# Kernel tuning notes

Measured on AMD Instinct MI355X. Metric: run time of the kernel, lower is better.

Reference implementation:

```python
import jax, jax.numpy as jnp
import numpy as np


def _hungarian(cost):
    """Jonker-Volgenant shortest-augmenting-path LAP solver (minimum cost).

    Returns col_ind such that rows arange(n) are matched to columns col_ind,
    identical (in objective) to scipy.optimize.linear_sum_assignment.
    Runs on host numpy, mirroring the original's detach().cpu() + scipy path.
    """
    cost = np.asarray(cost, dtype=np.float64)
    n = cost.shape[0]
    INF = np.inf
    u = np.zeros(n + 1)
    v = np.zeros(n + 1)
    p = np.zeros(n + 1, dtype=np.int64)   # p[j]: row (1-based) assigned to column j
    way = np.zeros(n + 1, dtype=np.int64)
    for i in range(1, n + 1):
        p[0] = i
        j0 = 0
        minv = np.full(n + 1, INF)
        used = np.zeros(n + 1, dtype=bool)
        while True:
            used[j0] = True
            i0 = p[j0]
            # vectorized relaxation of reduced costs for all unused columns
            cur = cost[i0 - 1] - u[i0] - v[1:]
            free = ~used[1:]
            upd = free & (cur < minv[1:])
            minv[1:] = np.where(upd, cur, minv[1:])
            way[1:] = np.where(upd, j0, way[1:])
            cand = np.where(free, minv[1:], INF)
            j1 = int(np.argmin(cand)) + 1
            delta = cand[j1 - 1]
            u[p[used]] += delta
            v[used] -= delta
            minv[1:] = np.where(free, minv[1:] - delta, minv[1:])
            j0 = j1
            if p[j0] == 0:
                break
        # augment along the alternating path
        while j0:
            j1 = way[j0]
            p[j0] = p[j1]
            j0 = j1
    col = np.empty(n, dtype=np.int64)
    col[p[1:] - 1] = np.arange(n)
    return col


def setup_inputs() -> dict:
    key = jax.random.key(0)
    B, N = 64, 256
    D = jax.random.normal(key, (B, N, N), dtype=jnp.float32)
    return {"D": D}


def reference(D):
    # Host round-trip for the assignment, exactly as the torch module does
    # (D.detach().cpu().numpy() -> scipy LAP per batch element).
    Dn = np.asarray(jax.device_get(D))
    cols = np.stack([_hungarian(Dn[b]) for b in range(Dn.shape[0])])  # [B, N]
    idx = jnp.asarray(cols)[:, :, None]                               # [B, N, 1]
    # gather matched costs D[b, i, col[b, i]] and reduce: mean per batch, then mean
    matched = jnp.take_along_axis(D, idx, axis=2)[..., 0]             # [B, N]
    return matched.mean(axis=1).mean()
```

## Files before the change

kernel.cpp:

```cpp
#include <hip/hip_runtime.h>
#include <hip/hip_fp16.h>

#define N_DIM 256
#define BATCH 64
#define BS 64

struct __align__(8) H4 { __half2 a, b; };

__device__ __forceinline__ unsigned fmap(float f) {
    unsigned b = __float_as_uint(f);
    return (b & 0x80000000u) ? ~b : (b | 0x80000000u);
}

#define DPP_MINU(x, ctrl) do {                                                 \
    unsigned _s = (unsigned)__builtin_amdgcn_update_dpp((int)(x), (int)(x),    \
                                                        (ctrl), 0xf, 0xf, false); \
    (x) = ((x) < _s) ? (x) : _s;                                               \
} while (0)

__device__ __forceinline__ unsigned wave_min_u32(unsigned x) {
    DPP_MINU(x, 0x111); DPP_MINU(x, 0x112); DPP_MINU(x, 0x114); DPP_MINU(x, 0x118);
    DPP_MINU(x, 0x142); DPP_MINU(x, 0x143);
    return (unsigned)__builtin_amdgcn_readlane((int)x, 63);
}

__device__ __forceinline__ int rd4_i(int x0, int x1, int x2, int x3, int idx) {
    const int sel = idx & 3, src = idx >> 2;
    int ab = (sel & 1) ? x1 : x0;
    int cd = (sel & 1) ? x3 : x2;
    int vv = (sel & 2) ? cd : ab;
    return __builtin_amdgcn_readlane(vv, src);
}
__device__ __forceinline__ float rd4_f(float x0, float x1, float x2, float x3, int idx) {
    return __int_as_float(rd4_i(__float_as_int(x0), __float_as_int(x1),
                                __float_as_int(x2), __float_as_int(x3), idx));
}

#define SET4(x0, x1, x2, x3, idx, val) do {                                    \
    const int _sel = (idx) & 3;                                                \
    if (t == ((idx) >> 2)) {                                                   \
        if (_sel == 0) x0 = (val); else if (_sel == 1) x1 = (val);             \
        else if (_sel == 2) x2 = (val); else x3 = (val);                       \
    }                                                                          \
} while (0)

__global__ __launch_bounds__(BS) void lap_kernel(const float* __restrict__ Dm,
                                                 double* __restrict__ batch_sums) {
    const int b = blockIdx.x;
    const int t = threadIdx.x;
    const float* __restrict__ cost = Dm + (size_t)b * N_DIM * N_DIM;
    const float4* __restrict__ cost4 = (const float4*)cost;

    __shared__ H4       ch[N_DIM * BS];
    __shared__ float    u_s[N_DIM];
    __shared__ float    v_s[N_DIM];
    __shared__ int      row4col_s[N_DIM];
    __shared__ int      col4row_s[N_DIM];
    __shared__ int      queue_s[N_DIM];
    __shared__ unsigned bid_s[N_DIM];
    __shared__ int      qcnt_s;

    const int c0i = 4 * t, c1i = 4 * t + 1, c2i = 4 * t + 2, c3i = 4 * t + 3;

    float cmn0 = INFINITY, cmn1 = INFINITY, cmn2 = INFINITY, cmn3 = INFINITY;
    int   ca0 = 0, ca1 = 0, ca2 = 0, ca3 = 0;
    for (int r = 0; r < N_DIM; ++r) {
        const float4 c4 = cost4[r * BS + t];
        H4 h;
        h.a = __floats2half2_rn(c4.x, c4.y);
        h.b = __floats2half2_rn(c4.z, c4.w);
        ch[r * BS + t] = h;
        const float r0 = __low2float(h.a), r1 = __high2float(h.a);
        const float r2 = __low2float(h.b), r3 = __high2float(h.b);
        if (r0 < cmn0) { cmn0 = r0; ca0 = r; }
        if (r1 < cmn1) { cmn1 = r1; ca1 = r; }
        if (r2 < cmn2) { cmn2 = r2; ca2 = r; }
        if (r3 < cmn3) { cmn3 = r3; ca3 = r; }
    }
    {
        float4 vv; vv.x = cmn0; vv.y = cmn1; vv.z = cmn2; vv.w = cmn3;
        ((float4*)v_s)[t] = vv;
        float4 zz; zz.x = 0.f; zz.y = 0.f; zz.z = 0.f; zz.w = 0.f;
        ((float4*)u_s)[t] = zz;
        int4 mm; mm.x = -1; mm.y = -1; mm.z = -1; mm.w = -1;
        ((int4*)row4col_s)[t] = mm;
        ((int4*)col4row_s)[t] = mm;
        int4 rc; rc.x = 0x7fffffff; rc.y = 0x7fffffff; rc.z = 0x7fffffff; rc.w = 0x7fffffff;
        ((int4*)queue_s)[t] = rc;
        uint4 bb; bb.x = ~0u; bb.y = ~0u; bb.z = ~0u; bb.w = ~0u;
        ((uint4*)bid_s)[t] = bb;
    }
    __syncthreads();
    atomicMin(&queue_s[ca0], c0i);
    atomicMin(&queue_s[ca1], c1i);
    atomicMin(&queue_s[ca2], c2i);
    atomicMin(&queue_s[ca3], c3i);
    __syncthreads();
    if (queue_s[ca0] == c0i) { row4col_s[c0i] = ca0; col4row_s[ca0] = c0i; }
    if (queue_s[ca1] == c1i) { row4col_s[c1i] = ca1; col4row_s[ca1] = c1i; }
    if (queue_s[ca2] == c2i) { row4col_s[c2i] = ca2; col4row_s[ca2] = c2i; }
    if (queue_s[ca3] == c3i) { row4col_s[c3i] = ca3; col4row_s[ca3] = c3i; }
    __syncthreads();

    for (int pass = 0; pass < 12; ++pass) {
        if (t == 0) qcnt_s = 0;
        __syncthreads();
        {
            const int4 my = ((const int4*)col4row_s)[t];
            const int nf = (my.x < 0) + (my.y < 0) + (my.z < 0) + (my.w < 0);
            if (nf) {
                int pos = atomicAdd(&qcnt_s, nf);
                if (my.x < 0) queue_s[pos++] = c0i;
                if (my.y < 0) queue_s[pos++] = c1i;
                if (my.z < 0) queue_s[pos++] = c2i;
                if (my.w < 0) queue_s[pos++] = c3i;
            }
        }
        __syncthreads();
        const int n = qcnt_s;
        if (n == 0) break;
        const int my_row = (t < n) ? queue_s[t] : -1;
        float d1 = INFINITY, d2 = INFINITY;
        int   j1 = 0;
        if (my_row >= 0) {
            const int base = my_row * BS;
            for (int l = 0; l < BS; ++l) {
                const int l2 = (l + t) & 63;
                const H4 h = ch[base + l2];
                const float4 vv = ((const float4*)v_s)[l2];
                float d;
                d = __low2float(h.a)  - vv.x; if (d < d1) { d2 = d1; d1 = d; j1 = 4 * l2 + 0; } else if (d < d2) d2 = d;
                d = __high2float(h.a) - vv.y; if (d < d1) { d2 = d1; d1 = d; j1 = 4 * l2 + 1; } else if (d < d2) d2 = d;
                d = __low2float(h.b)  - vv.z; if (d < d1) { d2 = d1; d1 = d; j1 = 4 * l2 + 2; } else if (d < d2) d2 = d;
                d = __high2float(h.b) - vv.w; if (d < d1) { d2 = d1; d1 = d; j1 = 4 * l2 + 3; } else if (d < d2) d2 = d;
            }
            atomicMin(&bid_s[j1], (fmap(d1) & 0xFFFFFF00u) | (unsigned)t);
        }
        __syncthreads();
        if (my_row >= 0) {
            const unsigned mybid = (fmap(d1) & 0xFFFFFF00u) | (unsigned)t;
            if (bid_s[j1] == mybid) {
                const int i0 = row4col_s[j1];
                row4col_s[j1] = my_row;
                col4row_s[my_row] = j1;
                if (i0 >= 0) col4row_s[i0] = -1;
                u_s[my_row] = d2;
                v_s[j1] += d1 - d2;
                bid_s[j1] = ~0u;
            }
        }
        __syncthreads();
    }

    const float4 vv4 = ((const float4*)v_s)[t];
    float v0 = vv4.x, v1 = vv4.y, v2 = vv4.z, v3 = vv4.w;
    const int4 m4 = ((const int4*)row4col_s)[t];
    int r4c0 = m4.x, r4c1 = m4.y, r4c2 = m4.z, r4c3 = m4.w;
    const int4 y4 = ((const int4*)col4row_s)[t];
    int c4r0 = y4.x, c4r1 = y4.y, c4r2 = y4.z, c4r3 = y4.w;
    int p0 = 0, p1 = 0, p2 = 0, p3 = 0;

    unsigned long long fm0 = __ballot(c4r0 < 0);
    unsigned long long fm1 = __ballot(c4r1 < 0);
    unsigned long long fm2 = __ballot(c4r2 < 0);
    unsigned long long fm3 = __ballot(c4r3 < 0);

    const unsigned KINF0 = (fmap(INFINITY) & 0xFFFFFF00u) | (unsigned)c0i;
    const unsigned KINF1 = (fmap(INFINITY) & 0xFFFFFF00u) | (unsigned)c1i;
    const unsigned KINF2 = (fmap(INFINITY) & 0xFFFFFF00u) | (unsigned)c2i;
    const unsigned KINF3 = (fmap(INFINITY) & 0xFFFFFF00u) | (unsigned)c3i;

    while (fm0 | fm1 | fm2 | fm3) {
        int i;
        if (fm0)      { const int tt = __builtin_ctzll(fm0); fm0 &= fm0 - 1; i = tt * 4 + 0; }
        else if (fm1) { const int tt = __builtin_ctzll(fm1); fm1 &= fm1 - 1; i = tt * 4 + 1; }
        else if (fm2) { const int tt = __builtin_ctzll(fm2); fm2 &= fm2 - 1; i = tt * 4 + 2; }
        else          { const int tt = __builtin_ctzll(fm3); fm3 &= fm3 - 1; i = tt * 4 + 3; }

        float spc0 = INFINITY, spc1 = INFINITY, spc2 = INFINITY, spc3 = INFINITY;
        unsigned key0 = KINF0, key1 = KINF1, key2 = KINF2, key3 = KINF3;
        int   scan = 0;
        int   cur = i;
        float minVal = 0.0f;
        int   sink = -1;

        while (true) {
            const H4    h = ch[cur * BS + t];
            const float ucur = u_s[cur];
            const float add = minVal - ucur;

            float r;
            r = add + __low2float(h.a)  - v0;
            if (r < spc0) { spc0 = r; p0 = cur; key0 = (fmap(r) & 0xFFFFFF00u) | (unsigned)c0i; }
            r = add + __high2float(h.a) - v1;
            if (r < spc1) { spc1 = r; p1 = cur; key1 = (fmap(r) & 0xFFFFFF00u) | (unsigned)c1i; }
            r = add + __low2float(h.b)  - v2;
            if (r < spc2) { spc2 = r; p2 = cur; key2 = (fmap(r) & 0xFFFFFF00u) | (unsigned)c2i; }
            r = add + __high2float(h.b) - v3;
            if (r < spc3) { spc3 = r; p3 = cur; key3 = (fmap(r) & 0xFFFFFF00u) | (unsigned)c3i; }

            unsigned k01 = (key0 < key1) ? key0 : key1;
            unsigned k23 = (key2 < key3) ? key2 : key3;
            const unsigned gk = wave_min_u32((k01 < k23) ? k01 : k23);
            const int bi = (int)(gk & 0xFFu);

            const float mv = rd4_f(spc0, spc1, spc2, spc3, bi);
            const int   r4 = rd4_i(r4c0, r4c1, r4c2, r4c3, bi);
            minVal = mv;
            if (t == (bi >> 2)) {
                const int s = bi & 3;
                scan |= 1 << s;
                if (s == 0) key0 = ~0u; else if (s == 1) key1 = ~0u;
                else if (s == 2) key2 = ~0u; else key3 = ~0u;
            }
            if (r4 < 0) { sink = bi; break; }
            cur = r4;
        }

        if (scan & 1) { const float dv = minVal - spc0; v0 -= dv; if (r4c0 >= 0) u_s[r4c0] += dv; }
        if (scan & 2) { const float dv = minVal - spc1; v1 -= dv; if (r4c1 >= 0) u_s[r4c1] += dv; }
        if (scan & 4) { const float dv = minVal - spc2; v2 -= dv; if (r4c2 >= 0) u_s[r4c2] += dv; }
        if (scan & 8) { const float dv = minVal - spc3; v3 -= dv; if (r4c3 >= 0) u_s[r4c3] += dv; }
        if (t == 0) u_s[i] += minVal;

        if (sink >= 0) {
            int jj = sink;
            while (true) {
                const int ii = rd4_i(p0, p1, p2, p3, jj);
                SET4(r4c0, r4c1, r4c2, r4c3, jj, ii);
                const int tmp = rd4_i(c4r0, c4r1, c4r2, c4r3, ii);
                SET4(c4r0, c4r1, c4r2, c4r3, ii, jj);
                jj = tmp;
                if (ii == i) break;
            }
        }
    }

    double s = 0.0;
    s += (double)cost[(size_t)(t * 4 + 0) * N_DIM + c4r0];
    s += (double)cost[(size_t)(t * 4 + 1) * N_DIM + c4r1];
    s += (double)cost[(size_t)(t * 4 + 2) * N_DIM + c4r2];
    s += (double)cost[(size_t)(t * 4 + 3) * N_DIM + c4r3];
    #pragma unroll
    for (int off = 32; off > 0; off >>= 1) s += __shfl_down(s, off);
    if (t == 0) batch_sums[b] = s;
}

__global__ void finalize_kernel(const double* __restrict__ batch_sums,
                                float* __restrict__ out) {
    const int t = threadIdx.x;
    double s = batch_sums[t];
    #pragma unroll
    for (int off = 32; off > 0; off >>= 1) s += __shfl_down(s, off);
    if (t == 0) out[0] = (float)(s / (double)((long long)BATCH * N_DIM));
}

extern "C" void kernel_launch(void* const* d_in, const int* in_sizes, int n_in,
                              void* d_out, int out_size, void* d_ws, size_t ws_size,
                              hipStream_t stream) {
    const float* Dm = (const float*)d_in[0];
    float* out = (float*)d_out;
    double* sums = (double*)d_ws;

    lap_kernel<<<BATCH, BS, 0, stream>>>(Dm, sums);
    finalize_kernel<<<1, 64, 0, stream>>>(sums, out);
}
```

Measured before the change: 906.8 us.

## Switch LAP solver to scaled 16-bit fixed-point integer costs and duals

Replaces the fp16 cost cache and float duals with costs scaled by 4096, rounded to int16 and packed in pairs, plus integer duals. The shortest-path inner loop now packs the reduced cost and column index into one integer key, so the per-step readlane of the min value and the fmap conversions go away. The auction pass now processes queued rows in chunks of 64 instead of only the first 64. It risks overflow or clipping for large costs and changes rounding versus the fp16 version, which could alter the chosen assignment.

```diff
diff --git a/kernel.cpp b/kernel.cpp
--- a/kernel.cpp
+++ b/kernel.cpp
@@ -1,16 +1,9 @@
 #include <hip/hip_runtime.h>
-#include <hip/hip_fp16.h>
 
 #define N_DIM 256
 #define BATCH 64
 #define BS 64
-
-struct __align__(8) H4 { __half2 a, b; };
-
-__device__ __forceinline__ unsigned fmap(float f) {
-    unsigned b = __float_as_uint(f);
-    return (b & 0x80000000u) ? ~b : (b | 0x80000000u);
-}
+#define SCALE 4096.0f
 
 #define DPP_MINU(x, ctrl) do {                                                 \
     unsigned _s = (unsigned)__builtin_amdgcn_update_dpp((int)(x), (int)(x),    \
@@ -30,10 +23,6 @@
     int cd = (sel & 1) ? x3 : x2;
     int vv = (sel & 2) ? cd : ab;
     return __builtin_amdgcn_readlane(vv, src);
-}
-__device__ __forceinline__ float rd4_f(float x0, float x1, float x2, float x3, int idx) {
-    return __int_as_float(rd4_i(__float_as_int(x0), __float_as_int(x1),
-                                __float_as_int(x2), __float_as_int(x3), idx));
 }
 
 #define SET4(x0, x1, x2, x3, idx, val) do {                                    \
@@ -44,6 +33,9 @@
     }                                                                          \
 } while (0)
 
+__device__ __forceinline__ int lo16(int p) { return (int)(short)(p & 0xFFFF); }
+__device__ __forceinline__ int hi16(int p) { return p >> 16; }
+
 __global__ __launch_bounds__(BS) void lap_kernel(const float* __restrict__ Dm,
                                                  double* __restrict__ batch_sums) {
     const int b = blockIdx.x;
@@ -51,9 +43,9 @@
     const float* __restrict__ cost = Dm + (size_t)b * N_DIM * N_DIM;
     const float4* __restrict__ cost4 = (const float4*)cost;
 
-    __shared__ H4       ch[N_DIM * BS];
-    __shared__ float    u_s[N_DIM];
-    __shared__ float    v_s[N_DIM];
+    __shared__ int2     chi[N_DIM * BS];
+    __shared__ int      u_s[N_DIM];
+    __shared__ int      v_s[N_DIM];
     __shared__ int      row4col_s[N_DIM];
     __shared__ int      col4row_s[N_DIM];
     __shared__ int      queue_s[N_DIM];
@@ -62,26 +54,28 @@
 
     const int c0i = 4 * t, c1i = 4 * t + 1, c2i = 4 * t + 2, c3i = 4 * t + 3;
 
-    float cmn0 = INFINITY, cmn1 = INFINITY, cmn2 = INFINITY, cmn3 = INFINITY;
-    int   ca0 = 0, ca1 = 0, ca2 = 0, ca3 = 0;
+    int cmn0 = INT_MAX, cmn1 = INT_MAX, cmn2 = INT_MAX, cmn3 = INT_MAX;
+    int ca0 = 0, ca1 = 0, ca2 = 0, ca3 = 0;
     for (int r = 0; r < N_DIM; ++r) {
         const float4 c4 = cost4[r * BS + t];
-        H4 h;
-        h.a = __floats2half2_rn(c4.x, c4.y);
-        h.b = __floats2half2_rn(c4.z, c4.w);
-        ch[r * BS + t] = h;
-        const float r0 = __low2float(h.a), r1 = __high2float(h.a);
-        const float r2 = __low2float(h.b), r3 = __high2float(h.b);
-        if (r0 < cmn0) { cmn0 = r0; ca0 = r; }
-        if (r1 < cmn1) { cmn1 = r1; ca1 = r; }
-        if (r2 < cmn2) { cmn2 = r2; ca2 = r; }
-        if (r3 < cmn3) { cmn3 = r3; ca3 = r; }
+        const int a0 = __float2int_rn(c4.x * SCALE);
+        const int a1 = __float2int_rn(c4.y * SCALE);
+        const int a2 = __float2int_rn(c4.z * SCALE);
+        const int a3 = __float2int_rn(c4.w * SCALE);
+        int2 p;
+        p.x = (a0 & 0xFFFF) | (a1 << 16);
+        p.y = (a2 & 0xFFFF) | (a3 << 16);
+        chi[r * BS + t] = p;
+        if (a0 < cmn0) { cmn0 = a0; ca0 = r; }
+        if (a1 < cmn1) { cmn1 = a1; ca1 = r; }
+        if (a2 < cmn2) { cmn2 = a2; ca2 = r; }
+        if (a3 < cmn3) { cmn3 = a3; ca3 = r; }
     }
     {
-        float4 vv; vv.x = cmn0; vv.y = cmn1; vv.z = cmn2; vv.w = cmn3;
-        ((float4*)v_s)[t] = vv;
-        float4 zz; zz.x = 0.f; zz.y = 0.f; zz.z = 0.f; zz.w = 0.f;
-        ((float4*)u_s)[t] = zz;
+        int4 vv; vv.x = cmn0; vv.y = cmn1; vv.z = cmn2; vv.w = cmn3;
+        ((int4*)v_s)[t] = vv;
+        int4 zz; zz.x = 0; zz.y = 0; zz.z = 0; zz.w = 0;
+        ((int4*)u_s)[t] = zz;
         int4 mm; mm.x = -1; mm.y = -1; mm.z = -1; mm.w = -1;
         ((int4*)row4col_s)[t] = mm;
         ((int4*)col4row_s)[t] = mm;
@@ -119,41 +113,43 @@
         __syncthreads();
         const int n = qcnt_s;
         if (n == 0) break;
-        const int my_row = (t < n) ? queue_s[t] : -1;
-        float d1 = INFINITY, d2 = INFINITY;
-        int   j1 = 0;
-        if (my_row >= 0) {
-            const int base = my_row * BS;
-            for (int l = 0; l < BS; ++l) {
-                const int l2 = (l + t) & 63;
-                const H4 h = ch[base + l2];
-                const float4 vv = ((const float4*)v_s)[l2];
-                float d;
-                d = __low2float(h.a)  - vv.x; if (d < d1) { d2 = d1; d1 = d; j1 = 4 * l2 + 0; } else if (d < d2) d2 = d;
-                d = __high2float(h.a) - vv.y; if (d < d1) { d2 = d1; d1 = d; j1 = 4 * l2 + 1; } else if (d < d2) d2 = d;
-                d = __low2float(h.b)  - vv.z; if (d < d1) { d2 = d1; d1 = d; j1 = 4 * l2 + 2; } else if (d < d2) d2 = d;
-                d = __high2float(h.b) - vv.w; if (d < d1) { d2 = d1; d1 = d; j1 = 4 * l2 + 3; } else if (d < d2) d2 = d;
-            }
-            atomicMin(&bid_s[j1], (fmap(d1) & 0xFFFFFF00u) | (unsigned)t);
-        }
-        __syncthreads();
-        if (my_row >= 0) {
-            const unsigned mybid = (fmap(d1) & 0xFFFFFF00u) | (unsigned)t;
-            if (bid_s[j1] == mybid) {
-                const int i0 = row4col_s[j1];
-                row4col_s[j1] = my_row;
-                col4row_s[my_row] = j1;
-                if (i0 >= 0) col4row_s[i0] = -1;
-                u_s[my_row] = d2;
-                v_s[j1] += d1 - d2;
-                bid_s[j1] = ~0u;
-            }
-        }
-        __syncthreads();
-    }
-
-    const float4 vv4 = ((const float4*)v_s)[t];
-    float v0 = vv4.x, v1 = vv4.y, v2 = vv4.z, v3 = vv4.w;
+        for (int base = 0; base < n; base += BS) {
+            const int my_row = (base + t < n) ? queue_s[base + t] : -1;
+            int d1 = INT_MAX, d2 = INT_MAX;
+            int j1 = 0;
+            if (my_row >= 0) {
+                const int rb = my_row * BS;
+                for (int l = 0; l < BS; ++l) {
+                    const int l2 = (l + t) & 63;
+                    const int2 h = chi[rb + l2];
+                    const int4 vv = ((const int4*)v_s)[l2];
+                    int d;
+                    d = lo16(h.x) - vv.x; if (d < d1) { d2 = d1; d1 = d; j1 = 4 * l2 + 0; } else if (d < d2) d2 = d;
+                    d = hi16(h.x) - vv.y; if (d < d1) { d2 = d1; d1 = d; j1 = 4 * l2 + 1; } else if (d < d2) d2 = d;
+                    d = lo16(h.y) - vv.z; if (d < d1) { d2 = d1; d1 = d; j1 = 4 * l2 + 2; } else if (d < d2) d2 = d;
+                    d = hi16(h.y) - vv.w; if (d < d1) { d2 = d1; d1 = d; j1 = 4 * l2 + 3; } else if (d < d2) d2 = d;
+                }
+                atomicMin(&bid_s[j1], ((unsigned)d1 << 8) | (unsigned)t);
+            }
+            __syncthreads();
+            if (my_row >= 0) {
+                const unsigned mybid = ((unsigned)d1 << 8) | (unsigned)t;
+                if (bid_s[j1] == mybid) {
+                    const int i0 = row4col_s[j1];
+                    row4col_s[j1] = my_row;
+                    col4row_s[my_row] = j1;
+                    if (i0 >= 0) col4row_s[i0] = -1;
+                    u_s[my_row] = d2;
+                    v_s[j1] += d1 - d2;
+                    bid_s[j1] = ~0u;
+                }
+            }
+            __syncthreads();
+        }
+    }
+
+    const int4 vv4 = ((const int4*)v_s)[t];
+    int vn0 = -vv4.x, vn1 = -vv4.y, vn2 = -vv4.z, vn3 = -vv4.w;
     const int4 m4 = ((const int4*)row4col_s)[t];
     int r4c0 = m4.x, r4c1 = m4.y, r4c2 = m4.z, r4c3 = m4.w;
     const int4 y4 = ((const int4*)col4row_s)[t];
@@ -165,10 +161,10 @@
     unsigned long long fm2 = __ballot(c4r2 < 0);
     unsigned long long fm3 = __ballot(c4r3 < 0);
 
-    const unsigned KINF0 = (fmap(INFINITY) & 0xFFFFFF00u) | (unsigned)c0i;
-    const unsigned KINF1 = (fmap(INFINITY) & 0xFFFFFF00u) | (unsigned)c1i;
-    const unsigned KINF2 = (fmap(INFINITY) & 0xFFFFFF00u) | (unsigned)c2i;
-    const unsigned KINF3 = (fmap(INFINITY) & 0xFFFFFF00u) | (unsigned)c3i;
+    const int KINIT0 = (0x7FFFFF << 8) | c0i;
+    const int KINIT1 = (0x7FFFFF << 8) | c1i;
+    const int KINIT2 = (0x7FFFFF << 8) | c2i;
+    const int KINIT3 = (0x7FFFFF << 8) | c3i;
 
     while (fm0 | fm1 | fm2 | fm3) {
         int i;
@@ -177,50 +173,48 @@
         else if (fm2) { const int tt = __builtin_ctzll(fm2); fm2 &= fm2 - 1; i = tt * 4 + 2; }
         else          { const int tt = __builtin_ctzll(fm3); fm3 &= fm3 - 1; i = tt * 4 + 3; }
 
-        float spc0 = INFINITY, spc1 = INFINITY, spc2 = INFINITY, spc3 = INFINITY;
-        unsigned key0 = KINF0, key1 = KINF1, key2 = KINF2, key3 = KINF3;
-        int   scan = 0;
-        int   cur = i;
-        float minVal = 0.0f;
-        int   sink = -1;
+        int k0 = KINIT0, k1 = KINIT1, k2 = KINIT2, k3 = KINIT3;
+        int g0 = 0, g1 = 0, g2 = 0, g3 = 0;
+        int cur = i;
+        int minVal = 0;
+        int sink = -1;
 
         while (true) {
-            const H4    h = ch[cur * BS + t];
-            const float ucur = u_s[cur];
-            const float add = minVal - ucur;
-
-            float r;
-            r = add + __low2float(h.a)  - v0;
-            if (r < spc0) { spc0 = r; p0 = cur; key0 = (fmap(r) & 0xFFFFFF00u) | (unsigned)c0i; }
-            r = add + __high2float(h.a) - v1;
-            if (r < spc1) { spc1 = r; p1 = cur; key1 = (fmap(r) & 0xFFFFFF00u) | (unsigned)c1i; }
-            r = add + __low2float(h.b)  - v2;
-            if (r < spc2) { spc2 = r; p2 = cur; key2 = (fmap(r) & 0xFFFFFF00u) | (unsigned)c2i; }
-            r = add + __high2float(h.b) - v3;
-            if (r < spc3) { spc3 = r; p3 = cur; key3 = (fmap(r) & 0xFFFFFF00u) | (unsigned)c3i; }
-
-            unsigned k01 = (key0 < key1) ? key0 : key1;
-            unsigned k23 = (key2 < key3) ? key2 : key3;
-            const unsigned gk = wave_min_u32((k01 < k23) ? k01 : k23);
-            const int bi = (int)(gk & 0xFFu);
-
-            const float mv = rd4_f(spc0, spc1, spc2, spc3, bi);
-            const int   r4 = rd4_i(r4c0, r4c1, r4c2, r4c3, bi);
-            minVal = mv;
+            const int2 h   = chi[cur * BS + t];
+            const int ucur = u_s[cur];
+            const int add  = minVal - ucur;
+
+            int r, kn;
+            r  = add + lo16(h.x) + vn0;
+            kn = (r << 8) | c0i; if (kn < k0) { p0 = cur; k0 = kn; }
+            r  = add + hi16(h.x) + vn1;
+            kn = (r << 8) | c1i; if (kn < k1) { p1 = cur; k1 = kn; }
+            r  = add + lo16(h.y) + vn2;
+            kn = (r << 8) | c2i; if (kn < k2) { p2 = cur; k2 = kn; }
+            r  = add + hi16(h.y) + vn3;
+            kn = (r << 8) | c3i; if (kn < k3) { p3 = cur; k3 = kn; }
+
+            const int q0 = k0 | g0, q1 = k1 | g1, q2 = k2 | g2, q3 = k3 | g3;
+            int q01 = (q0 < q1) ? q0 : q1;
+            int q23 = (q2 < q3) ? q2 : q3;
+            const int gk = (int)wave_min_u32((unsigned)((q01 < q23) ? q01 : q23));
+
+            const int bi = gk & 0xFF;
+            minVal = gk >> 8;
+            const int r4 = rd4_i(r4c0, r4c1, r4c2, r4c3, bi);
             if (t == (bi >> 2)) {
                 const int s = bi & 3;
-                scan |= 1 << s;
-                if (s == 0) key0 = ~0u; else if (s == 1) key1 = ~0u;
-                else if (s == 2) key2 = ~0u; else key3 = ~0u;
+                if (s == 0) g0 = 0x7FFFFFFF; else if (s == 1) g1 = 0x7FFFFFFF;
+                else if (s == 2) g2 = 0x7FFFFFFF; else g3 = 0x7FFFFFFF;
             }
             if (r4 < 0) { sink = bi; break; }
             cur = r4;
         }
 
-        if (scan & 1) { const float dv = minVal - spc0; v0 -= dv; if (r4c0 >= 0) u_s[r4c0] += dv; }
-        if (scan & 2) { const float dv = minVal - spc1; v1 -= dv; if (r4c1 >= 0) u_s[r4c1] += dv; }
-        if (scan & 4) { const float dv = minVal - spc2; v2 -= dv; if (r4c2 >= 0) u_s[r4c2] += dv; }
-        if (scan & 8) { const float dv = minVal - spc3; v3 -= dv; if (r4c3 >= 0) u_s[r4c3] += dv; }
+        if (g0) { const int dv = minVal - (k0 >> 8); vn0 += dv; if (r4c0 >= 0) u_s[r4c0] += dv; }
+        if (g1) { const int dv = minVal - (k1 >> 8); vn1 += dv; if (r4c1 >= 0) u_s[r4c1] += dv; }
+        if (g2) { const int dv = minVal - (k2 >> 8); vn2 += dv; if (r4c2 >= 0) u_s[r4c2] += dv; }
+        if (g3) { const int dv = minVal - (k3 >> 8); vn3 += dv; if (r4c3 >= 0) u_s[r4c3] += dv; }
         if (t == 0) u_s[i] += minVal;
 
         if (sink >= 0) {
```

After: 754.8 us. 16.8% less time.
